# Kernel tuning notes

Hardware: AMD Instinct MI355X
Metric: run time of the kernel (lower is better)

## Reference

```python
import jax, jax.numpy as jnp
import numpy as np

EPS = 1e-5
K = 3  # deformable conv kernel size


def _conv2d_same(x, w, b=None):
    # x (N,C,H,W), w (O,I,kh,kw), stride 1, SAME padding
    y = jax.lax.conv_general_dilated(
        x, w, window_strides=(1, 1), padding='SAME',
        dimension_numbers=('NCHW', 'OIHW', 'NCHW'))
    if b is not None:
        y = y + b[None, :, None, None]
    return y


def _bilinear_sample(x, ys, xs):
    # x (N,C,H,W); ys, xs (N,H,W) float sample coords -> (N,C,H,W), zero pad outside
    N, C, H, W = x.shape
    y0 = jnp.floor(ys)
    x0 = jnp.floor(xs)
    dy = ys - y0
    dx = xs - x0
    xf = x.reshape(N, C, H * W)

    def gather(yi, xi):
        valid = (yi >= 0) & (yi < H) & (xi >= 0) & (xi < W)
        yc = jnp.clip(yi, 0, H - 1).astype(jnp.int32)
        xc = jnp.clip(xi, 0, W - 1).astype(jnp.int32)
        idx = (yc * W + xc).reshape(N, 1, H * W)
        v = jnp.take_along_axis(xf, jnp.broadcast_to(idx, (N, C, H * W)), axis=2)
        return v.reshape(N, C, H, W) * valid[:, None].astype(x.dtype)

    v00 = gather(y0, x0)
    v01 = gather(y0, x0 + 1)
    v10 = gather(y0 + 1, x0)
    v11 = gather(y0 + 1, x0 + 1)
    dy = dy[:, None]
    dx = dx[:, None]
    return (v00 * (1 - dy) * (1 - dx) + v01 * (1 - dy) * dx
            + v10 * dy * (1 - dx) + v11 * dy * dx)


def _dcn_v2(x, w_off, b_off, w, b):
    # Modulated deformable conv (DCNv2), 3x3, stride 1, pad 1
    N, Cin, H, W = x.shape
    om = _conv2d_same(x, w_off, b_off)              # (N, 3*K*K, H, W)
    o1, o2, m = jnp.split(om, 3, axis=1)
    off = jnp.concatenate([o1, o2], axis=1)          # (N, 2*K*K, H, W)
    mask = jax.nn.sigmoid(m)                         # (N, K*K, H, W)
    base_y = jnp.arange(H, dtype=x.dtype)[None, :, None]  # (1,H,1)
    base_x = jnp.arange(W, dtype=x.dtype)[None, None, :]  # (1,1,W)
    out = jnp.broadcast_to(b[None, :, None, None], (N, w.shape[0], H, W)).astype(x.dtype)
    for k in range(K * K):  # fixed small loop over kernel taps
        ki, kj = k // K, k % K
        ys = base_y + (ki - 1) + off[:, 2 * k]
        xs = base_x + (kj - 1) + off[:, 2 * k + 1]
        v = _bilinear_sample(x, ys, xs) * mask[:, k][:, None]
        out = out + jnp.einsum('nchw,oc->nohw', v, w[:, :, ki, kj])
    return out


def _batchnorm(x, gamma, beta):
    # training-mode BN over (N,H,W)
    mu = x.mean(axis=(0, 2, 3), keepdims=True)
    var = x.var(axis=(0, 2, 3), keepdims=True)
    xhat = (x - mu) * jax.lax.rsqrt(var + EPS)
    return xhat * gamma[None, :, None, None] + beta[None, :, None, None]


def _conv_transpose2d(x, w):
    # torch ConvTranspose2d(k=4, s=2, p=1, bias=False); w (Cin, Cout, 4, 4)
    kernel = jnp.flip(w, (2, 3)).transpose(1, 0, 2, 3)  # (Cout, Cin, 4, 4)
    return jax.lax.conv_general_dilated(
        x, kernel, window_strides=(1, 1),
        padding=((2, 2), (2, 2)), lhs_dilation=(2, 2),
        dimension_numbers=('NCHW', 'OIHW', 'NCHW'))


def setup_inputs() -> dict:
    key = jax.random.key(0)
    ks = jax.random.split(key, 9)
    N, inC, outC, H, W = 8, 256, 256, 64, 64
    x = jax.random.normal(ks[0], (N, inC, H, W), dtype=jnp.float32)
    w_off = jax.random.normal(ks[1], (3 * K * K, inC, K, K), dtype=jnp.float32) * 0.01
    b_off = jnp.zeros((3 * K * K,), dtype=jnp.float32)
    w_dcn = jax.random.normal(ks[2], (outC, inC, K, K), dtype=jnp.float32) * (1.0 / np.sqrt(inC * K * K))
    b_dcn = jnp.zeros((outC,), dtype=jnp.float32)
    gamma1 = jnp.ones((outC,), dtype=jnp.float32)
    beta1 = jnp.zeros((outC,), dtype=jnp.float32)
    w_ct = jax.random.normal(ks[3], (outC, outC, 4, 4), dtype=jnp.float32) * (1.0 / np.sqrt(outC * 16))
    gamma2 = jnp.ones((outC,), dtype=jnp.float32)
    beta2 = jnp.zeros((outC,), dtype=jnp.float32)
    return {'x': x, 'w_off': w_off, 'b_off': b_off, 'w_dcn': w_dcn,
            'b_dcn': b_dcn, 'gamma1': gamma1, 'beta1': beta1,
            'w_ct': w_ct, 'gamma2': gamma2, 'beta2': beta2}


def reference(x, w_off, b_off, w_dcn, b_dcn, gamma1, beta1, w_ct, gamma2, beta2):
    out = _dcn_v2(x, w_off, b_off, w_dcn, b_dcn)
    out = jax.nn.relu(_batchnorm(out, gamma1, beta1))
    out = _conv_transpose2d(out, w_ct)
    out = jax.nn.relu(_batchnorm(out, gamma2, beta2))
    return out  # (N, outC, 2H, 2W)
```

## Files before the change

kernel.cpp:

```cpp
#include <hip/hip_runtime.h>


#define OFF_XT   0u
#define SZ_XT    (8u*64u*64u*256u)
#define OFF_Y1   (OFF_XT + SZ_XT)
#define SZ_Y1    SZ_XT
#define OFF_OM   (OFF_Y1 + SZ_Y1)
#define SZ_OM    (8u*27u*4096u)
#define OFF_WD   (OFF_OM + SZ_OM)
#define SZ_WD    (9u*256u*256u)
#define OFF_WC   (OFF_WD + SZ_WD)
#define SZ_WC    (16u*256u*256u)
#define OFF_WO   (OFF_WC + 524288u)
#define OFF_ST   (OFF_WC + SZ_WC)
#define OFF_P1   (OFF_ST + 2048u)

typedef __attribute__((ext_vector_type(8))) short bf16x8;
typedef __attribute__((ext_vector_type(4))) float f32x4;

__device__ __forceinline__ unsigned short f2bf(float f) {
  unsigned int u = __float_as_uint(f);
  u += 0x7fffu + ((u >> 16) & 1u);
  return (unsigned short)(u >> 16);
}

__device__ __forceinline__ unsigned int lerp_pair(unsigned int u00, unsigned int u01,
                                                  unsigned int u10, unsigned int u11,
                                                  float w0, float w1, float w2, float w3) {
  float lo = w0 * __uint_as_float(u00 << 16) + w1 * __uint_as_float(u01 << 16) +
             w2 * __uint_as_float(u10 << 16) + w3 * __uint_as_float(u11 << 16);
  float hi = w0 * __uint_as_float(u00 & 0xffff0000u) + w1 * __uint_as_float(u01 & 0xffff0000u) +
             w2 * __uint_as_float(u10 & 0xffff0000u) + w3 * __uint_as_float(u11 & 0xffff0000u);
  return (unsigned int)f2bf(lo) | ((unsigned int)f2bf(hi) << 16);
}

__global__ __launch_bounds__(256) void k_transpose_x(const float* __restrict__ x,
                                                     unsigned short* __restrict__ xtb) {
  __shared__ float tile[32][33];
  int ny = blockIdx.x;
  int n = ny >> 6, y = ny & 63;
  int c0 = blockIdx.y * 32;
  int w0 = blockIdx.z * 32;
  int t = threadIdx.x;
  int tx = t & 31, ty = t >> 5;
#pragma unroll
  for (int i = 0; i < 4; ++i) {
    int c = c0 + ty + i * 8;
    tile[ty + i * 8][tx] = x[(((n * 256 + c) * 64 + y) << 6) + w0 + tx];
  }
  __syncthreads();
#pragma unroll
  for (int i = 0; i < 4; ++i) {
    int wl = ty + i * 8;
    xtb[(((n * 64 + y) * 64 + (w0 + wl)) << 8) + c0 + tx] = f2bf(tile[tx][wl]);
  }
}

__global__ void k_prep_wdcn(const float* __restrict__ w, unsigned short* __restrict__ wdb) {
  int idx = blockIdx.x * 256 + threadIdx.x;
  if (idx < 589824) {
    int cil = idx & 31;
    int co = (idx >> 5) & 255;
    int chunk = (idx >> 13) & 7;
    int k = idx >> 16;
    int ci = chunk * 32 + cil;
    wdb[idx] = f2bf(w[(co * 256 + ci) * 9 + k]);
  }
}

__global__ void k_prep_wct(const float* __restrict__ w, unsigned short* __restrict__ wcb) {
  int idx = blockIdx.x * 256 + threadIdx.x;
  int cil = idx & 31;
  int co = (idx >> 5) & 255;
  int chunk = (idx >> 13) & 7;
  int tap = (idx >> 16) & 3;
  int px = (idx >> 18) & 1;
  int py = (idx >> 19) & 1;
  int ci = chunk * 32 + cil;
  int krA = (py == 0) ? 3 : 2, krB = (py == 0) ? 1 : 0;
  int kc0 = (px == 0) ? 3 : 2, kc1 = kc0 - 2;
  int kr = (tap < 2) ? krA : krB;
  int kc = (tap & 1) ? kc1 : kc0;
  float v = w[(ci << 12) + (co << 4) + kr * 4 + kc];
  wcb[idx] = f2bf(v);
}

__global__ void k_prep_woff(const float* __restrict__ w, unsigned short* __restrict__ wob) {
  int idx = blockIdx.x * 256 + threadIdx.x;
  int cil = idx & 31;
  int co = (idx >> 5) & 31;
  int chunk = (idx >> 10) & 7;
  int tap = idx >> 13;
  int ci = chunk * 32 + cil;
  float v = (co < 27) ? w[(co * 256 + ci) * 9 + tap] : 0.f;
  wob[idx] = f2bf(v);
}

__global__ __launch_bounds__(512) void k_offset_mfma(const unsigned short* __restrict__ xtb,
                                                     const unsigned short* __restrict__ wob,
                                                     const float* __restrict__ b_off,
                                                     float* __restrict__ om) {
  __shared__ unsigned short aLds[6 * 66 * 40];
  __shared__ unsigned short wLds[9 * 32 * 40];
  int bid = blockIdx.x;
  int n = bid & 7, yq = bid >> 3;
  int ybase = yq * 4;
  int t = threadIdx.x;
  int wave = t >> 6, lane = t & 63;
  int lr = wave >> 1, cb = (wave & 1) * 32;
  int l15 = lane & 15, l4 = lane >> 4;
  f32x4 acc[2][2] = {};

  for (int chunk = 0; chunk < 8; ++chunk) {
    __syncthreads();
    for (int task = t; task < 1584; task += 512) {
      int slot = task & 3;
      int rc = task >> 2;
      int c = rc % 66, r = rc / 66;
      int gy = ybase - 1 + r, gx = c - 1;
      uint4 val = make_uint4(0u, 0u, 0u, 0u);
      if (gy >= 0 && gy < 64 && gx >= 0 && gx < 64)
        val = *(const uint4*)&xtb[((size_t)(n * 4096 + gy * 64 + gx) << 8) + chunk * 32 + slot * 8];
      *(uint4*)&aLds[(r * 66 + c) * 40 + slot * 8] = val;
    }
    for (int task = t; task < 1152; task += 512) {
      int sl = task & 3;
      int co = (task >> 2) & 31;
      int tap = task >> 7;
      *(uint4*)&wLds[(tap * 32 + co) * 40 + sl * 8] =
          *(const uint4*)&wob[(size_t)((tap * 8 + chunk) * 32 + co) * 32 + sl * 8];
    }
    __syncthreads();
#pragma unroll
    for (int ky = 0; ky < 3; ++ky)
#pragma unroll
      for (int kx = 0; kx < 3; ++kx) {
        int tap = ky * 3 + kx;
        bf16x8 b0 = *(bf16x8*)&wLds[(tap * 32 + l15) * 40 + l4 * 8];
        bf16x8 b1 = *(bf16x8*)&wLds[(tap * 32 + 16 + l15) * 40 + l4 * 8];
        bf16x8 a0 = *(bf16x8*)&aLds[((lr + ky) * 66 + cb + l15 + kx) * 40 + l4 * 8];
        bf16x8 a1 = *(bf16x8*)&aLds[((lr + ky) * 66 + cb + 16 + l15 + kx) * 40 + l4 * 8];
        acc[0][0] = __builtin_amdgcn_mfma_f32_16x16x32_bf16(a0, b0, acc[0][0], 0, 0, 0);
        acc[0][1] = __builtin_amdgcn_mfma_f32_16x16x32_bf16(a0, b1, acc[0][1], 0, 0, 0);
        acc[1][0] = __builtin_amdgcn_mfma_f32_16x16x32_bf16(a1, b0, acc[1][0], 0, 0, 0);
        acc[1][1] = __builtin_amdgcn_mfma_f32_16x16x32_bf16(a1, b1, acc[1][1], 0, 0, 0);
      }
  }
  int row = ybase + lr;
#pragma unroll
  for (int j = 0; j < 2; ++j) {
    int co = 16 * j + l15;
    if (co < 27) {
      float bias = b_off[co];
      float* dst = om + ((size_t)(n * 27 + co) << 12) + row * 64;
#pragma unroll
      for (int i = 0; i < 2; ++i) {
        f32x4 v = acc[i][j];
        float4 o = make_float4(v[0] + bias, v[1] + bias, v[2] + bias, v[3] + bias);
        *(float4*)&dst[cb + 16 * i + l4 * 4] = o;
      }
    }
  }
}

__global__ __launch_bounds__(512) void k_dcn2(const unsigned short* __restrict__ xtb,
                                              const float* __restrict__ om,
                                              const unsigned short* __restrict__ wdb,
                                              const float* __restrict__ b_dcn,
                                              unsigned short* __restrict__ y1r,
                                              float* __restrict__ part1) {
  __shared__ unsigned short aLds[128 * 40];
  __shared__ int p_yx[1152];
  __shared__ float p_w[1152 * 4];
  __shared__ float sstat[512];
  int bid = blockIdx.x;
  int n = bid & 7, yp = bid >> 3;
  int ybase = yp * 2;
  int t = threadIdx.x;
  int wave = t >> 6, lane = t & 63;
  int mh = wave >> 2, ns = wave & 3;
  int l15 = lane & 15, l4 = lane >> 4;
  int gp = t >> 2, gq = t & 3;
  int nb = n << 12;
  f32x4 acc[4][4] = {};

  for (int i = t; i < 1152; i += 512) {
    int tap = i >> 7, pp = i & 127;
    int ki = tap / 3, kj = tap % 3;
    int yy = ybase + (pp >> 6), xx = pp & 63;
    const float* base = om + (n * 27) * 4096 + (yy << 6) + xx;
    float offy = base[(2 * tap) * 4096];
    float offx = base[(2 * tap + 1) * 4096];
    float mv = base[(18 + tap) * 4096];
    float mask = 1.f / (1.f + expf(-mv));
    float ysf = (float)(yy + ki - 1) + offy;
    float xsf = (float)(xx + kj - 1) + offx;
    float y0f = floorf(ysf), x0f = floorf(xsf);
    float dy = ysf - y0f, dx = xsf - x0f;
    int y0 = (int)y0f, x0 = (int)x0f;
    int y1c = y0 + 1, x1c = x0 + 1;
    float v00 = (y0 >= 0 && y0 < 64 && x0 >= 0 && x0 < 64) ? 1.f : 0.f;
    float v01 = (y0 >= 0 && y0 < 64 && x1c >= 0 && x1c < 64) ? 1.f : 0.f;
    float v10 = (y1c >= 0 && y1c < 64 && x0 >= 0 && x0 < 64) ? 1.f : 0.f;
    float v11 = (y1c >= 0 && y1c < 64 && x1c >= 0 && x1c < 64) ? 1.f : 0.f;
    int cy0 = min(max(y0, 0), 63), cy1 = min(max(y1c, 0), 63);
    int cx0 = min(max(x0, 0), 63), cx1 = min(max(x1c, 0), 63);
    p_yx[i] = cy0 | (cy1 << 8) | (cx0 << 16) | (cx1 << 24);
    p_w[i * 4 + 0] = (1.f - dy) * (1.f - dx) * mask * v00;
    p_w[i * 4 + 1] = (1.f - dy) * dx * mask * v01;
    p_w[i * 4 + 2] = dy * (1.f - dx) * mask * v10;
    p_w[i * 4 + 3] = dy * dx * mask * v11;
  }
  __syncthreads();

  const unsigned short *b00, *b01, *b10, *b11;
  float w0, w1, w2, w3;
#define LOADP(TAP_)                                                                   \
  {                                                                                   \
    int ii = (TAP_) * 128 + gp;                                                       \
    int pk = p_yx[ii];                                                                \
    int y0 = pk & 255, y1c = (pk >> 8) & 255, x0 = (pk >> 16) & 255, x1c = pk >> 24;  \
    w0 = p_w[ii * 4 + 0]; w1 = p_w[ii * 4 + 1];                                       \
    w2 = p_w[ii * 4 + 2]; w3 = p_w[ii * 4 + 3];                                       \
    b00 = xtb + ((size_t)(nb + (y0 << 6) + x0) << 8) + gq * 8;                        \
    b01 = xtb + ((size_t)(nb + (y0 << 6) + x1c) << 8) + gq * 8;                       \
    b10 = xtb + ((size_t)(nb + (y1c << 6) + x0) << 8) + gq * 8;                       \
    b11 = xtb + ((size_t)(nb + (y1c << 6) + x1c) << 8) + gq * 8;                      \
  }
  uint4 g00, g01, g10, g11;
  LOADP(0);
  g00 = *(const uint4*)(b00); g01 = *(const uint4*)(b01);
  g10 = *(const uint4*)(b10); g11 = *(const uint4*)(b11);

  for (int tap = 0; tap < 9; ++tap) {
    for (int chunk = 0; chunk < 8; ++chunk) {
      __syncthreads();
      {
        uint4 o;
        o.x = lerp_pair(g00.x, g01.x, g10.x, g11.x, w0, w1, w2, w3);
        o.y = lerp_pair(g00.y, g01.y, g10.y, g11.y, w0, w1, w2, w3);
        o.z = lerp_pair(g00.z, g01.z, g10.z, g11.z, w0, w1, w2, w3);
        o.w = lerp_pair(g00.w, g01.w, g10.w, g11.w, w0, w1, w2, w3);
        *(uint4*)&aLds[gp * 40 + gq * 8] = o;
      }
      if (!(tap == 8 && chunk == 7)) {
        int ntap = tap, nchunk = chunk + 1;
        if (nchunk == 8) { nchunk = 0; ntap = tap + 1; LOADP(ntap); }
        int cio = nchunk * 32;
        g00 = *(const uint4*)(b00 + cio); g01 = *(const uint4*)(b01 + cio);
        g10 = *(const uint4*)(b10 + cio); g11 = *(const uint4*)(b11 + cio);
      }
      __syncthreads();
      const unsigned short* wp = wdb + (size_t)tap * 65536 + chunk * 8192;
      bf16x8 b[4], a[4];
#pragma unroll
      for (int j = 0; j < 4; ++j)
        b[j] = *(bf16x8*)&wp[(ns * 64 + 16 * j + l15) * 32 + l4 * 8];
#pragma unroll
      for (int i = 0; i < 4; ++i)
        a[i] = *(bf16x8*)&aLds[(mh * 64 + 16 * i + l15) * 40 + l4 * 8];
#pragma unroll
      for (int i = 0; i < 4; ++i)
#pragma unroll
        for (int j = 0; j < 4; ++j)
          acc[i][j] = __builtin_amdgcn_mfma_f32_16x16x32_bf16(a[i], b[j], acc[i][j], 0, 0, 0);
    }
  }
#undef LOADP
  sstat[t] = 0.f;
  __syncthreads();
  unsigned short* dst = y1r + ((size_t)(n * 4096 + ybase * 64) << 8);
#pragma unroll
  for (int j = 0; j < 4; ++j) {
    int co = ns * 64 + 16 * j + l15;
    float bias = b_dcn[co];
    float ss = 0.f, qq = 0.f;
#pragma unroll
    for (int i = 0; i < 4; ++i)
#pragma unroll
      for (int rr = 0; rr < 4; ++rr) {
        int pos = mh * 64 + 16 * i + l4 * 4 + rr;
        float v = acc[i][j][rr] + bias;
        dst[pos * 256 + co] = f2bf(v);
        ss += v; qq += v * v;
      }
    ss += __shfl_xor(ss, 16); ss += __shfl_xor(ss, 32);
    qq += __shfl_xor(qq, 16); qq += __shfl_xor(qq, 32);
    if (l4 == 0) { atomicAdd(&sstat[co], ss); atomicAdd(&sstat[256 + co], qq); }
  }
  __syncthreads();
  part1[(size_t)bid * 512 + t] = sstat[t];
}

__global__ __launch_bounds__(256) void k_finalize_p(const float* __restrict__ part,
                                                    const float* __restrict__ gamma,
                                                    const float* __restrict__ beta,
                                                    float* __restrict__ scsh,
                                                    float inv_cnt, int nblocks) {
  __shared__ float red[512];
  int c = blockIdx.x;
  int t = threadIdx.x;
  float s = 0.f, q = 0.f;
  for (int b = t; b < nblocks; b += 256) {
    s += part[(size_t)b * 512 + c];
    q += part[(size_t)b * 512 + 256 + c];
  }
  red[t] = s;
  red[256 + t] = q;
  __syncthreads();
  for (int w = 128; w > 0; w >>= 1) {
    if (t < w) { red[t] += red[t + w]; red[256 + t] += red[256 + t + w]; }
    __syncthreads();
  }
  if (t == 0) {
    float mu = red[0] * inv_cnt;
    float var = red[256] * inv_cnt - mu * mu;
    float r = rsqrtf(var + 1e-5f);
    float sc = gamma[c] * r;
    scsh[c] = sc;
    scsh[256 + c] = beta[c] - mu * sc;
  }
}

__global__ void k_norm_b16(unsigned short* __restrict__ y1r, const float* __restrict__ scsh) {
  int idx = blockIdx.x * 256 + threadIdx.x;
  int cb = (idx & 31) * 8;
  uint4 v = *(uint4*)&y1r[(size_t)idx * 8];
  float4 sc0 = *(const float4*)&scsh[cb];
  float4 sc1 = *(const float4*)&scsh[cb + 4];
  float4 sh0 = *(const float4*)&scsh[256 + cb];
  float4 sh1 = *(const float4*)&scsh[256 + cb + 4];
  float f0 = __uint_as_float(v.x << 16), f1 = __uint_as_float(v.x & 0xffff0000u);
  float f2 = __uint_as_float(v.y << 16), f3 = __uint_as_float(v.y & 0xffff0000u);
  float f4 = __uint_as_float(v.z << 16), f5 = __uint_as_float(v.z & 0xffff0000u);
  float f6 = __uint_as_float(v.w << 16), f7 = __uint_as_float(v.w & 0xffff0000u);
  f0 = fmaxf(fmaf(f0, sc0.x, sh0.x), 0.f); f1 = fmaxf(fmaf(f1, sc0.y, sh0.y), 0.f);
  f2 = fmaxf(fmaf(f2, sc0.z, sh0.z), 0.f); f3 = fmaxf(fmaf(f3, sc0.w, sh0.w), 0.f);
  f4 = fmaxf(fmaf(f4, sc1.x, sh1.x), 0.f); f5 = fmaxf(fmaf(f5, sc1.y, sh1.y), 0.f);
  f6 = fmaxf(fmaf(f6, sc1.z, sh1.z), 0.f); f7 = fmaxf(fmaf(f7, sc1.w, sh1.w), 0.f);
  uint4 o;
  o.x = (unsigned int)f2bf(f0) | ((unsigned int)f2bf(f1) << 16);
  o.y = (unsigned int)f2bf(f2) | ((unsigned int)f2bf(f3) << 16);
  o.z = (unsigned int)f2bf(f4) | ((unsigned int)f2bf(f5) << 16);
  o.w = (unsigned int)f2bf(f6) | ((unsigned int)f2bf(f7) << 16);
  *(uint4*)&y1r[(size_t)idx * 8] = o;
}

__global__ __launch_bounds__(512) void k_convt2(const unsigned short* __restrict__ y1b,
                                               const unsigned short* __restrict__ wcb,
                                               float* __restrict__ out,
                                               float* __restrict__ part2) {
  __shared__ unsigned short sh[16896];
  __shared__ float sstat[512];
  unsigned short* aLds = sh;

  int bid = blockIdx.x;
  int n = bid & 7;
  int r2 = bid >> 3;
  int py = r2 & 1;
  int ub = r2 >> 1;
  int u0 = ub * 2;
  int ry0 = u0 - 1 + py;
  int t = threadIdx.x;
  int wave = t >> 6, lane = t & 63;
  int px_w = wave >> 2, ns = wave & 3;
  int co_base = ns * 64;
  int l15 = lane & 15, l4 = lane >> 4;
  bool rvalid[3];
#pragma unroll
  for (int r = 0; r < 3; ++r) rvalid[r] = (ry0 + r >= 0) && (ry0 + r < 64);

  f32x4 acc[2][4][4] = {};

  for (int chunk = 0; chunk < 8; ++chunk) {
    int ci0 = chunk * 32;
    __syncthreads();
    for (int task = t; task < 792; task += 512) {
      int slot = task & 3;
      int rc = task >> 2;
      int c = rc % 66;
      int r = rc / 66;
      int ix = c - 1;
      uint4 val = make_uint4(0u, 0u, 0u, 0u);
      if (rvalid[r] && ix >= 0 && ix < 64)
        val = *(const uint4*)&y1b[((size_t)(n * 4096 + (ry0 + r) * 64 + ix) * 256 + ci0 + slot * 8)];
      *(uint4*)&aLds[(r * 66 + c) * 40 + slot * 8] = val;
    }
    __syncthreads();
    for (int tap = 0; tap < 4; ++tap) {
      int r_ofs = tap >> 1, s = tap & 1;
      const unsigned short* wsrc =
          wcb + ((size_t)((((py * 2 + px_w) * 4 + tap) * 8 + chunk) * 256 + co_base)) * 32;
      bf16x8 b[4];
#pragma unroll
      for (int j = 0; j < 4; ++j)
        b[j] = *(bf16x8*)&wsrc[(16 * j + l15) * 32 + l4 * 8];
#pragma unroll
      for (int k = 0; k < 2; ++k)
#pragma unroll
        for (int i = 0; i < 4; ++i) {
          int c = 16 * i + l15 + s + px_w;
          bf16x8 a = *(bf16x8*)&aLds[((k + r_ofs) * 66 + c) * 40 + l4 * 8];
#pragma unroll
          for (int j = 0; j < 4; ++j)
            acc[k][i][j] = __builtin_amdgcn_mfma_f32_16x16x32_bf16(a, b[j], acc[k][i][j], 0, 0, 0);
        }
    }
  }

  sstat[t] = 0.f;
  float* epi = (float*)sh;
#pragma unroll
  for (int k = 0; k < 2; ++k) {
    int oy = 2 * (u0 + k) + py;
    for (int qt = 0; qt < 4; ++qt) {
      __syncthreads();
      if (ns == qt) {
#pragma unroll
        for (int i = 0; i < 4; ++i)
#pragma unroll
          for (int j = 0; j < 4; ++j) {
            int co_l = 16 * j + l15;
            int vbase = 16 * i + l4 * 4;
            *(f32x4*)&epi[co_l * 132 + px_w * 64 + vbase] = acc[k][i][j];
          }
      }
      __syncthreads();
#pragma unroll
      for (int it = 0; it < 4; ++it) {
        int task = it * 512 + t;
        int q = task & 31;
        int co_l = task >> 5;
        int co = qt * 64 + co_l;
        float e00 = epi[co_l * 132 + 2 * q];
        float e01 = epi[co_l * 132 + 2 * q + 1];
        float e10 = epi[co_l * 132 + 64 + 2 * q];
        float e11 = epi[co_l * 132 + 64 + 2 * q + 1];
        float4 vv = make_float4(e00, e10, e01, e11);
        *(float4*)&out[((size_t)(n * 256 + co) * 128 + oy) * 128 + 4 * q] = vv;
        float ss = e00 + e01 + e10 + e11;
        float qq = e00 * e00 + e01 * e01 + e10 * e10 + e11 * e11;
        ss += __shfl_xor(ss, 1);  qq += __shfl_xor(qq, 1);
        ss += __shfl_xor(ss, 2);  qq += __shfl_xor(qq, 2);
        ss += __shfl_xor(ss, 4);  qq += __shfl_xor(qq, 4);
        ss += __shfl_xor(ss, 8);  qq += __shfl_xor(qq, 8);
        ss += __shfl_xor(ss, 16); qq += __shfl_xor(qq, 16);
        if ((lane & 31) == 0) {
          atomicAdd(&sstat[co], ss);
          atomicAdd(&sstat[256 + co], qq);
        }
      }
    }
  }
  __syncthreads();
  part2[(size_t)bid * 512 + t] = sstat[t];
}

__global__ void k_norm_nchw(float* __restrict__ buf, const float* __restrict__ scsh) {
  int idx = blockIdx.x * 256 + threadIdx.x;
  int c = (idx >> 12) & 255;
  float sc = scsh[c], sh = scsh[256 + c];
  float4 v = *(float4*)&buf[(size_t)idx * 4];
  v.x = fmaxf(fmaf(v.x, sc, sh), 0.f);
  v.y = fmaxf(fmaf(v.y, sc, sh), 0.f);
  v.z = fmaxf(fmaf(v.z, sc, sh), 0.f);
  v.w = fmaxf(fmaf(v.w, sc, sh), 0.f);
  *(float4*)&buf[(size_t)idx * 4] = v;
}

extern "C" void kernel_launch(void* const* d_in, const int* in_sizes, int n_in,
                              void* d_out, int out_size, void* d_ws, size_t ws_size,
                              hipStream_t stream) {
  (void)in_sizes; (void)n_in; (void)out_size; (void)ws_size;
  const float* x      = (const float*)d_in[0];
  const float* w_off  = (const float*)d_in[1];
  const float* b_off  = (const float*)d_in[2];
  const float* w_dcn  = (const float*)d_in[3];
  const float* b_dcn  = (const float*)d_in[4];
  const float* gamma1 = (const float*)d_in[5];
  const float* beta1  = (const float*)d_in[6];
  const float* w_ct   = (const float*)d_in[7];
  const float* gamma2 = (const float*)d_in[8];
  const float* beta2  = (const float*)d_in[9];
  float* ws  = (float*)d_ws;
  unsigned short* xtb = (unsigned short*)(ws + OFF_XT);
  unsigned short* y1r = (unsigned short*)(ws + OFF_Y1);
  float* om  = ws + OFF_OM;
  unsigned short* wdb = (unsigned short*)(ws + OFF_WD);
  unsigned short* wcb = (unsigned short*)(ws + OFF_WC);
  unsigned short* wob = (unsigned short*)(ws + OFF_WO);
  float* st  = ws + OFF_ST;
  float* p1  = ws + OFF_P1;
  float* out = (float*)d_out;

  k_transpose_x<<<dim3(512, 8, 2), 256, 0, stream>>>(x, xtb);
  k_prep_wdcn<<<2304, 256, 0, stream>>>(w_dcn, wdb);
  k_prep_wct<<<4096, 256, 0, stream>>>(w_ct, wcb);
  k_prep_woff<<<288, 256, 0, stream>>>(w_off, wob);
  k_offset_mfma<<<128, 512, 0, stream>>>(xtb, wob, b_off, om);
  k_dcn2<<<256, 512, 0, stream>>>(xtb, om, wdb, b_dcn, y1r, p1);
  k_finalize_p<<<256, 256, 0, stream>>>(p1, gamma1, beta1, st + 512, 1.f / 32768.f, 256);
  k_norm_b16<<<4096, 256, 0, stream>>>(y1r, st + 512);
  k_convt2<<<512, 512, 0, stream>>>(y1r, wcb, out, om);
  k_finalize_p<<<256, 256, 0, stream>>>(om, gamma2, beta2, st + 1536, 1.f / 131072.f, 512);
  k_norm_nchw<<<32768, 256, 0, stream>>>(out, st + 1536);
}
```

Before: 281.5 us.

## Fuse BN1+ReLU into convT loader and halve DCN block rows

Removes the separate k_norm_b16 pass by applying BN1 scale/shift and ReLU while k_convt2 loads y1 into LDS. k_dcn2 now handles one output row per block instead of two, doubling the grid to 512 blocks with smaller tiles and 8-byte gathers per thread. The partial-stats buffer is relocated to fit the larger block count. This saves a full read/write pass over the bf16 intermediate and raises parallelism in the DCN kernel, at the cost of less weight reuse per block and redundant normalization math across halo rows in the convT loader.

```diff
diff --git a/kernel.cpp b/kernel.cpp
--- a/kernel.cpp
+++ b/kernel.cpp
@@ -12,8 +12,8 @@
 #define OFF_WC   (OFF_WD + SZ_WD)
 #define SZ_WC    (16u*256u*256u)
 #define OFF_WO   (OFF_WC + 524288u)
+#define OFF_P1   (OFF_WC + 565248u)
 #define OFF_ST   (OFF_WC + SZ_WC)
-#define OFF_P1   (OFF_ST + 2048u)
 
 typedef __attribute__((ext_vector_type(8))) short bf16x8;
 typedef __attribute__((ext_vector_type(4))) float f32x4;
@@ -31,6 +31,13 @@
              w2 * __uint_as_float(u10 << 16) + w3 * __uint_as_float(u11 << 16);
   float hi = w0 * __uint_as_float(u00 & 0xffff0000u) + w1 * __uint_as_float(u01 & 0xffff0000u) +
              w2 * __uint_as_float(u10 & 0xffff0000u) + w3 * __uint_as_float(u11 & 0xffff0000u);
+  return (unsigned int)f2bf(lo) | ((unsigned int)f2bf(hi) << 16);
+}
+
+__device__ __forceinline__ unsigned int norm_pair(unsigned int u, float scx, float shx,
+                                                  float scy, float shy) {
+  float lo = fmaxf(fmaf(__uint_as_float(u << 16), scx, shx), 0.f);
+  float hi = fmaxf(fmaf(__uint_as_float(u & 0xffff0000u), scy, shy), 0.f);
   return (unsigned int)f2bf(lo) | ((unsigned int)f2bf(hi) << 16);
 }
 
@@ -169,32 +176,30 @@
                                               const float* __restrict__ b_dcn,
                                               unsigned short* __restrict__ y1r,
                                               float* __restrict__ part1) {
-  __shared__ unsigned short aLds[128 * 40];
-  __shared__ int p_yx[1152];
-  __shared__ float p_w[1152 * 4];
+  __shared__ unsigned short aLds[64 * 40];
+  __shared__ int p_yx[576];
+  __shared__ float p_w[576 * 4];
   __shared__ float sstat[512];
   int bid = blockIdx.x;
-  int n = bid & 7, yp = bid >> 3;
-  int ybase = yp * 2;
+  int n = bid & 7, y = bid >> 3;
   int t = threadIdx.x;
   int wave = t >> 6, lane = t & 63;
   int mh = wave >> 2, ns = wave & 3;
   int l15 = lane & 15, l4 = lane >> 4;
-  int gp = t >> 2, gq = t & 3;
+  int gp = t >> 3, gq = t & 7;
   int nb = n << 12;
-  f32x4 acc[4][4] = {};
-
-  for (int i = t; i < 1152; i += 512) {
-    int tap = i >> 7, pp = i & 127;
+  f32x4 acc[2][4] = {};
+
+  for (int i = t; i < 576; i += 512) {
+    int tap = i >> 6, pp = i & 63;
     int ki = tap / 3, kj = tap % 3;
-    int yy = ybase + (pp >> 6), xx = pp & 63;
-    const float* base = om + (n * 27) * 4096 + (yy << 6) + xx;
+    const float* base = om + (n * 27) * 4096 + (y << 6) + pp;
     float offy = base[(2 * tap) * 4096];
     float offx = base[(2 * tap + 1) * 4096];
     float mv = base[(18 + tap) * 4096];
     float mask = 1.f / (1.f + expf(-mv));
-    float ysf = (float)(yy + ki - 1) + offy;
-    float xsf = (float)(xx + kj - 1) + offx;
+    float ysf = (float)(y + ki - 1) + offy;
+    float xsf = (float)(pp + kj - 1) + offx;
     float y0f = floorf(ysf), x0f = floorf(xsf);
     float dy = ysf - y0f, dx = xsf - x0f;
     int y0 = (int)y0f, x0 = (int)x0f;
@@ -217,50 +222,48 @@
   float w0, w1, w2, w3;
 #define LOADP(TAP_)                                                                   \
   {                                                                                   \
-    int ii = (TAP_) * 128 + gp;                                                       \
+    int ii = (TAP_) * 64 + gp;                                                        \
     int pk = p_yx[ii];                                                                \
     int y0 = pk & 255, y1c = (pk >> 8) & 255, x0 = (pk >> 16) & 255, x1c = pk >> 24;  \
     w0 = p_w[ii * 4 + 0]; w1 = p_w[ii * 4 + 1];                                       \
     w2 = p_w[ii * 4 + 2]; w3 = p_w[ii * 4 + 3];                                       \
-    b00 = xtb + ((size_t)(nb + (y0 << 6) + x0) << 8) + gq * 8;                        \
-    b01 = xtb + ((size_t)(nb + (y0 << 6) + x1c) << 8) + gq * 8;                       \
-    b10 = xtb + ((size_t)(nb + (y1c << 6) + x0) << 8) + gq * 8;                       \
-    b11 = xtb + ((size_t)(nb + (y1c << 6) + x1c) << 8) + gq * 8;                      \
-  }
-  uint4 g00, g01, g10, g11;
+    b00 = xtb + ((size_t)(nb + (y0 << 6) + x0) << 8) + gq * 4;                        \
+    b01 = xtb + ((size_t)(nb + (y0 << 6) + x1c) << 8) + gq * 4;                       \
+    b10 = xtb + ((size_t)(nb + (y1c << 6) + x0) << 8) + gq * 4;                       \
+    b11 = xtb + ((size_t)(nb + (y1c << 6) + x1c) << 8) + gq * 4;                      \
+  }
+  uint2 g00, g01, g10, g11;
   LOADP(0);
-  g00 = *(const uint4*)(b00); g01 = *(const uint4*)(b01);
-  g10 = *(const uint4*)(b10); g11 = *(const uint4*)(b11);
+  g00 = *(const uint2*)(b00); g01 = *(const uint2*)(b01);
+  g10 = *(const uint2*)(b10); g11 = *(const uint2*)(b11);
 
   for (int tap = 0; tap < 9; ++tap) {
     for (int chunk = 0; chunk < 8; ++chunk) {
       __syncthreads();
       {
-        uint4 o;
+        uint2 o;
         o.x = lerp_pair(g00.x, g01.x, g10.x, g11.x, w0, w1, w2, w3);
         o.y = lerp_pair(g00.y, g01.y, g10.y, g11.y, w0, w1, w2, w3);
-        o.z = lerp_pair(g00.z, g01.z, g10.z, g11.z, w0, w1, w2, w3);
-        o.w = lerp_pair(g00.w, g01.w, g10.w, g11.w, w0, w1, w2, w3);
-        *(uint4*)&aLds[gp * 40 + gq * 8] = o;
+        *(uint2*)&aLds[gp * 40 + gq * 4] = o;
       }
       if (!(tap == 8 && chunk == 7)) {
         int ntap = tap, nchunk = chunk + 1;
         if (nchunk == 8) { nchunk = 0; ntap = tap + 1; LOADP(ntap); }
         int cio = nchunk * 32;
-        g00 = *(const uint4*)(b00 + cio); g01 = *(const uint4*)(b01 + cio);
-        g10 = *(const uint4*)(b10 + cio); g11 = *(const uint4*)(b11 + cio);
+        g00 = *(const uint2*)(b00 + cio); g01 = *(const uint2*)(b01 + cio);
+        g10 = *(const uint2*)(b10 + cio); g11 = *(const uint2*)(b11 + cio);
       }
       __syncthreads();
       const unsigned short* wp = wdb + (size_t)tap * 65536 + chunk * 8192;
-      bf16x8 b[4], a[4];
+      bf16x8 b[4], a[2];
 #pragma unroll
       for (int j = 0; j < 4; ++j)
         b[j] = *(bf16x8*)&wp[(ns * 64 + 16 * j + l15) * 32 + l4 * 8];
 #pragma unroll
-      for (int i = 0; i < 4; ++i)
-        a[i] = *(bf16x8*)&aLds[(mh * 64 + 16 * i + l15) * 40 + l4 * 8];
-#pragma unroll
-      for (int i = 0; i < 4; ++i)
+      for (int i = 0; i < 2; ++i)
+        a[i] = *(bf16x8*)&aLds[(mh * 32 + 16 * i + l15) * 40 + l4 * 8];
+#pragma unroll
+      for (int i = 0; i < 2; ++i)
 #pragma unroll
         for (int j = 0; j < 4; ++j)
           acc[i][j] = __builtin_amdgcn_mfma_f32_16x16x32_bf16(a[i], b[j], acc[i][j], 0, 0, 0);
@@ -269,17 +272,17 @@
 #undef LOADP
   sstat[t] = 0.f;
   __syncthreads();
-  unsigned short* dst = y1r + ((size_t)(n * 4096 + ybase * 64) << 8);
+  unsigned short* dst = y1r + ((size_t)(n * 4096 + y * 64) << 8);
 #pragma unroll
   for (int j = 0; j < 4; ++j) {
     int co = ns * 64 + 16 * j + l15;
     float bias = b_dcn[co];
     float ss = 0.f, qq = 0.f;
 #pragma unroll
-    for (int i = 0; i < 4; ++i)
+    for (int i = 0; i < 2; ++i)
 #pragma unroll
       for (int rr = 0; rr < 4; ++rr) {
-        int pos = mh * 64 + 16 * i + l4 * 4 + rr;
+        int pos = mh * 32 + 16 * i + l4 * 4 + rr;
         float v = acc[i][j][rr] + bias;
         dst[pos * 256 + co] = f2bf(v);
         ss += v; qq += v * v;
@@ -322,32 +325,9 @@
   }
 }
 
-__global__ void k_norm_b16(unsigned short* __restrict__ y1r, const float* __restrict__ scsh) {
-  int idx = blockIdx.x * 256 + threadIdx.x;
-  int cb = (idx & 31) * 8;
-  uint4 v = *(uint4*)&y1r[(size_t)idx * 8];
-  float4 sc0 = *(const float4*)&scsh[cb];
-  float4 sc1 = *(const float4*)&scsh[cb + 4];
-  float4 sh0 = *(const float4*)&scsh[256 + cb];
-  float4 sh1 = *(const float4*)&scsh[256 + cb + 4];
-  float f0 = __uint_as_float(v.x << 16), f1 = __uint_as_float(v.x & 0xffff0000u);
-  float f2 = __uint_as_float(v.y << 16), f3 = __uint_as_float(v.y & 0xffff0000u);
-  float f4 = __uint_as_float(v.z << 16), f5 = __uint_as_float(v.z & 0xffff0000u);
-  float f6 = __uint_as_float(v.w << 16), f7 = __uint_as_float(v.w & 0xffff0000u);
-  f0 = fmaxf(fmaf(f0, sc0.x, sh0.x), 0.f); f1 = fmaxf(fmaf(f1, sc0.y, sh0.y), 0.f);
-  f2 = fmaxf(fmaf(f2, sc0.z, sh0.z), 0.f); f3 = fmaxf(fmaf(f3, sc0.w, sh0.w), 0.f);
-  f4 = fmaxf(fmaf(f4, sc1.x, sh1.x), 0.f); f5 = fmaxf(fmaf(f5, sc1.y, sh1.y), 0.f);
-  f6 = fmaxf(fmaf(f6, sc1.z, sh1.z), 0.f); f7 = fmaxf(fmaf(f7, sc1.w, sh1.w), 0.f);
-  uint4 o;
-  o.x = (unsigned int)f2bf(f0) | ((unsigned int)f2bf(f1) << 16);
-  o.y = (unsigned int)f2bf(f2) | ((unsigned int)f2bf(f3) << 16);
-  o.z = (unsigned int)f2bf(f4) | ((unsigned int)f2bf(f5) << 16);
-  o.w = (unsigned int)f2bf(f6) | ((unsigned int)f2bf(f7) << 16);
-  *(uint4*)&y1r[(size_t)idx * 8] = o;
-}
-
 __global__ __launch_bounds__(512) void k_convt2(const unsigned short* __restrict__ y1b,
                                                const unsigned short* __restrict__ wcb,
+                                               const float* __restrict__ scsh1,
                                                float* __restrict__ out,
                                                float* __restrict__ part2) {
   __shared__ unsigned short sh[16896];
@@ -382,8 +362,18 @@
       int r = rc / 66;
       int ix = c - 1;
       uint4 val = make_uint4(0u, 0u, 0u, 0u);
-      if (rvalid[r] && ix >= 0 && ix < 64)
-        val = *(const uint4*)&y1b[((size_t)(n * 4096 + (ry0 + r) * 64 + ix) * 256 + ci0 + slot * 8)];
+      if (rvalid[r] && ix >= 0 && ix < 64) {
+        uint4 raw = *(const uint4*)&y1b[((size_t)(n * 4096 + (ry0 + r) * 64 + ix) * 256 + ci0 + slot * 8)];
+        int cb = ci0 + slot * 8;
+        float4 sc0 = *(const float4*)&scsh1[cb];
+        float4 sc1 = *(const float4*)&scsh1[cb + 4];
+        float4 sh0 = *(const float4*)&scsh1[256 + cb];
+        float4 sh1 = *(const float4*)&scsh1[256 + cb + 4];
+        val.x = norm_pair(raw.x, sc0.x, sh0.x, sc0.y, sh0.y);
+        val.y = norm_pair(raw.y, sc0.z, sh0.z, sc0.w, sh0.w);
+        val.z = norm_pair(raw.z, sc1.x, sh1.x, sc1.y, sh1.y);
+        val.w = norm_pair(raw.w, sc1.z, sh1.z, sc1.w, sh1.w);
+      }
       *(uint4*)&aLds[(r * 66 + c) * 40 + slot * 8] = val;
     }
     __syncthreads();
@@ -498,10 +488,9 @@
   k_prep_wct<<<4096, 256, 0, stream>>>(w_ct, wcb);
   k_prep_woff<<<288, 256, 0, stream>>>(w_off, wob);
   k_offset_mfma<<<128, 512, 0, stream>>>(xtb, wob, b_off, om);
-  k_dcn2<<<256, 512, 0, stream>>>(xtb, om, wdb, b_dcn, y1r, p1);
-  k_finalize_p<<<256, 256, 0, stream>>>(p1, gamma1, beta1, st + 512, 1.f / 32768.f, 256);
-  k_norm_b16<<<4096, 256, 0, stream>>>(y1r, st + 512);
-  k_convt2<<<512, 512, 0, stream>>>(y1r, wcb, out, om);
+  k_dcn2<<<512, 512, 0, stream>>>(xtb, om, wdb, b_dcn, y1r, p1);
+  k_finalize_p<<<256, 256, 0, stream>>>(p1, gamma1, beta1, st + 512, 1.f / 32768.f, 512);
+  k_convt2<<<512, 512, 0, stream>>>(y1r, wcb, st + 512, out, om);
   k_finalize_p<<<256, 256, 0, stream>>>(om, gamma2, beta2, st + 1536, 1.f / 131072.f, 512);
   k_norm_nchw<<<32768, 256, 0, stream>>>(out, st + 1536);
 }
```

After: 294.2 us. 4.5% more time.

## Double-buffer DCN A tile and fuse BN1+ReLU into conv-transpose loads

Applied to the files above, without the earlier changes.

Gives the DCN GEMM's A tile two LDS buffers, so each step computes the next bilinear tile while MFMAs consume the current one, dropping one barrier per iteration. Removes the standalone BN1+ReLU kernel and applies scale, shift and ReLU while loading y1 into LDS in the conv-transpose kernel. This saves a full read and write pass over the y1 intermediate and a launch, but repeats the normalisation for rows shared between the overlapping tiles. The P1 partial buffer is moved to a new workspace offset.

```diff
diff --git a/kernel.cpp b/kernel.cpp
--- a/kernel.cpp
+++ b/kernel.cpp
@@ -12,8 +12,8 @@
 #define OFF_WC   (OFF_WD + SZ_WD)
 #define SZ_WC    (16u*256u*256u)
 #define OFF_WO   (OFF_WC + 524288u)
+#define OFF_P1   (OFF_WC + 565248u)
 #define OFF_ST   (OFF_WC + SZ_WC)
-#define OFF_P1   (OFF_ST + 2048u)
 
 typedef __attribute__((ext_vector_type(8))) short bf16x8;
 typedef __attribute__((ext_vector_type(4))) float f32x4;
@@ -31,6 +31,13 @@
              w2 * __uint_as_float(u10 << 16) + w3 * __uint_as_float(u11 << 16);
   float hi = w0 * __uint_as_float(u00 & 0xffff0000u) + w1 * __uint_as_float(u01 & 0xffff0000u) +
              w2 * __uint_as_float(u10 & 0xffff0000u) + w3 * __uint_as_float(u11 & 0xffff0000u);
+  return (unsigned int)f2bf(lo) | ((unsigned int)f2bf(hi) << 16);
+}
+
+__device__ __forceinline__ unsigned int norm_pair(unsigned int u, float scx, float shx,
+                                                  float scy, float shy) {
+  float lo = fmaxf(fmaf(__uint_as_float(u << 16), scx, shx), 0.f);
+  float hi = fmaxf(fmaf(__uint_as_float(u & 0xffff0000u), scy, shy), 0.f);
   return (unsigned int)f2bf(lo) | ((unsigned int)f2bf(hi) << 16);
 }
 
@@ -169,7 +176,7 @@
                                               const float* __restrict__ b_dcn,
                                               unsigned short* __restrict__ y1r,
                                               float* __restrict__ part1) {
-  __shared__ unsigned short aLds[128 * 40];
+  __shared__ unsigned short aLds[2][128 * 40];
   __shared__ int p_yx[1152];
   __shared__ float p_w[1152 * 4];
   __shared__ float sstat[512];
@@ -227,46 +234,55 @@
     b10 = xtb + ((size_t)(nb + (y1c << 6) + x0) << 8) + gq * 8;                       \
     b11 = xtb + ((size_t)(nb + (y1c << 6) + x1c) << 8) + gq * 8;                      \
   }
+#define WRITE_A(BUF_)                                                                 \
+  {                                                                                   \
+    uint4 o;                                                                          \
+    o.x = lerp_pair(g00.x, g01.x, g10.x, g11.x, w0, w1, w2, w3);                      \
+    o.y = lerp_pair(g00.y, g01.y, g10.y, g11.y, w0, w1, w2, w3);                      \
+    o.z = lerp_pair(g00.z, g01.z, g10.z, g11.z, w0, w1, w2, w3);                      \
+    o.w = lerp_pair(g00.w, g01.w, g10.w, g11.w, w0, w1, w2, w3);                      \
+    *(uint4*)&aLds[BUF_][gp * 40 + gq * 8] = o;                                       \
+  }
   uint4 g00, g01, g10, g11;
   LOADP(0);
   g00 = *(const uint4*)(b00); g01 = *(const uint4*)(b01);
   g10 = *(const uint4*)(b10); g11 = *(const uint4*)(b11);
-
-  for (int tap = 0; tap < 9; ++tap) {
-    for (int chunk = 0; chunk < 8; ++chunk) {
-      __syncthreads();
-      {
-        uint4 o;
-        o.x = lerp_pair(g00.x, g01.x, g10.x, g11.x, w0, w1, w2, w3);
-        o.y = lerp_pair(g00.y, g01.y, g10.y, g11.y, w0, w1, w2, w3);
-        o.z = lerp_pair(g00.z, g01.z, g10.z, g11.z, w0, w1, w2, w3);
-        o.w = lerp_pair(g00.w, g01.w, g10.w, g11.w, w0, w1, w2, w3);
-        *(uint4*)&aLds[gp * 40 + gq * 8] = o;
-      }
-      if (!(tap == 8 && chunk == 7)) {
-        int ntap = tap, nchunk = chunk + 1;
-        if (nchunk == 8) { nchunk = 0; ntap = tap + 1; LOADP(ntap); }
-        int cio = nchunk * 32;
+  WRITE_A(0);
+  g00 = *(const uint4*)(b00 + 32); g01 = *(const uint4*)(b01 + 32);
+  g10 = *(const uint4*)(b10 + 32); g11 = *(const uint4*)(b11 + 32);
+  __syncthreads();
+
+  for (int p = 0; p < 72; ++p) {
+    int cur = p & 1;
+    int tap = p >> 3, chunk = p & 7;
+    const unsigned short* wp = wdb + (size_t)tap * 65536 + chunk * 8192;
+    bf16x8 b[4], a[4];
+#pragma unroll
+    for (int j = 0; j < 4; ++j)
+      b[j] = *(bf16x8*)&wp[(ns * 64 + 16 * j + l15) * 32 + l4 * 8];
+#pragma unroll
+    for (int i = 0; i < 4; ++i)
+      a[i] = *(bf16x8*)&aLds[cur][(mh * 64 + 16 * i + l15) * 40 + l4 * 8];
+#pragma unroll
+    for (int i = 0; i < 4; ++i)
+#pragma unroll
+      for (int j = 0; j < 4; ++j)
+        acc[i][j] = __builtin_amdgcn_mfma_f32_16x16x32_bf16(a[i], b[j], acc[i][j], 0, 0, 0);
+    if (p < 71) {
+      WRITE_A(cur ^ 1);
+      int q = p + 2;
+      if (q < 72) {
+        int qt = q >> 3, qc = q & 7;
+        if (qc == 0) LOADP(qt);
+        int cio = qc * 32;
         g00 = *(const uint4*)(b00 + cio); g01 = *(const uint4*)(b01 + cio);
         g10 = *(const uint4*)(b10 + cio); g11 = *(const uint4*)(b11 + cio);
       }
-      __syncthreads();
-      const unsigned short* wp = wdb + (size_t)tap * 65536 + chunk * 8192;
-      bf16x8 b[4], a[4];
-#pragma unroll
-      for (int j = 0; j < 4; ++j)
-        b[j] = *(bf16x8*)&wp[(ns * 64 + 16 * j + l15) * 32 + l4 * 8];
-#pragma unroll
-      for (int i = 0; i < 4; ++i)
-        a[i] = *(bf16x8*)&aLds[(mh * 64 + 16 * i + l15) * 40 + l4 * 8];
-#pragma unroll
-      for (int i = 0; i < 4; ++i)
-#pragma unroll
-        for (int j = 0; j < 4; ++j)
-          acc[i][j] = __builtin_amdgcn_mfma_f32_16x16x32_bf16(a[i], b[j], acc[i][j], 0, 0, 0);
-    }
+    }
+    __syncthreads();
   }
 #undef LOADP
+#undef WRITE_A
   sstat[t] = 0.f;
   __syncthreads();
   unsigned short* dst = y1r + ((size_t)(n * 4096 + ybase * 64) << 8);
@@ -322,32 +338,9 @@
   }
 }
 
-__global__ void k_norm_b16(unsigned short* __restrict__ y1r, const float* __restrict__ scsh) {
-  int idx = blockIdx.x * 256 + threadIdx.x;
-  int cb = (idx & 31) * 8;
-  uint4 v = *(uint4*)&y1r[(size_t)idx * 8];
-  float4 sc0 = *(const float4*)&scsh[cb];
-  float4 sc1 = *(const float4*)&scsh[cb + 4];
-  float4 sh0 = *(const float4*)&scsh[256 + cb];
-  float4 sh1 = *(const float4*)&scsh[256 + cb + 4];
-  float f0 = __uint_as_float(v.x << 16), f1 = __uint_as_float(v.x & 0xffff0000u);
-  float f2 = __uint_as_float(v.y << 16), f3 = __uint_as_float(v.y & 0xffff0000u);
-  float f4 = __uint_as_float(v.z << 16), f5 = __uint_as_float(v.z & 0xffff0000u);
-  float f6 = __uint_as_float(v.w << 16), f7 = __uint_as_float(v.w & 0xffff0000u);
-  f0 = fmaxf(fmaf(f0, sc0.x, sh0.x), 0.f); f1 = fmaxf(fmaf(f1, sc0.y, sh0.y), 0.f);
-  f2 = fmaxf(fmaf(f2, sc0.z, sh0.z), 0.f); f3 = fmaxf(fmaf(f3, sc0.w, sh0.w), 0.f);
-  f4 = fmaxf(fmaf(f4, sc1.x, sh1.x), 0.f); f5 = fmaxf(fmaf(f5, sc1.y, sh1.y), 0.f);
-  f6 = fmaxf(fmaf(f6, sc1.z, sh1.z), 0.f); f7 = fmaxf(fmaf(f7, sc1.w, sh1.w), 0.f);
-  uint4 o;
-  o.x = (unsigned int)f2bf(f0) | ((unsigned int)f2bf(f1) << 16);
-  o.y = (unsigned int)f2bf(f2) | ((unsigned int)f2bf(f3) << 16);
-  o.z = (unsigned int)f2bf(f4) | ((unsigned int)f2bf(f5) << 16);
-  o.w = (unsigned int)f2bf(f6) | ((unsigned int)f2bf(f7) << 16);
-  *(uint4*)&y1r[(size_t)idx * 8] = o;
-}
-
 __global__ __launch_bounds__(512) void k_convt2(const unsigned short* __restrict__ y1b,
                                                const unsigned short* __restrict__ wcb,
+                                               const float* __restrict__ scsh1,
                                                float* __restrict__ out,
                                                float* __restrict__ part2) {
   __shared__ unsigned short sh[16896];
@@ -382,8 +375,18 @@
       int r = rc / 66;
       int ix = c - 1;
       uint4 val = make_uint4(0u, 0u, 0u, 0u);
-      if (rvalid[r] && ix >= 0 && ix < 64)
-        val = *(const uint4*)&y1b[((size_t)(n * 4096 + (ry0 + r) * 64 + ix) * 256 + ci0 + slot * 8)];
+      if (rvalid[r] && ix >= 0 && ix < 64) {
+        uint4 raw = *(const uint4*)&y1b[((size_t)(n * 4096 + (ry0 + r) * 64 + ix) * 256 + ci0 + slot * 8)];
+        int cb = ci0 + slot * 8;
+        float4 sc0 = *(const float4*)&scsh1[cb];
+        float4 sc1 = *(const float4*)&scsh1[cb + 4];
+        float4 sh0 = *(const float4*)&scsh1[256 + cb];
+        float4 sh1 = *(const float4*)&scsh1[256 + cb + 4];
+        val.x = norm_pair(raw.x, sc0.x, sh0.x, sc0.y, sh0.y);
+        val.y = norm_pair(raw.y, sc0.z, sh0.z, sc0.w, sh0.w);
+        val.z = norm_pair(raw.z, sc1.x, sh1.x, sc1.y, sh1.y);
+        val.w = norm_pair(raw.w, sc1.z, sh1.z, sc1.w, sh1.w);
+      }
       *(uint4*)&aLds[(r * 66 + c) * 40 + slot * 8] = val;
     }
     __syncthreads();
@@ -500,8 +503,7 @@
   k_offset_mfma<<<128, 512, 0, stream>>>(xtb, wob, b_off, om);
   k_dcn2<<<256, 512, 0, stream>>>(xtb, om, wdb, b_dcn, y1r, p1);
   k_finalize_p<<<256, 256, 0, stream>>>(p1, gamma1, beta1, st + 512, 1.f / 32768.f, 256);
-  k_norm_b16<<<4096, 256, 0, stream>>>(y1r, st + 512);
-  k_convt2<<<512, 512, 0, stream>>>(y1r, wcb, out, om);
+  k_convt2<<<512, 512, 0, stream>>>(y1r, wcb, st + 512, out, om);
   k_finalize_p<<<256, 256, 0, stream>>>(om, gamma2, beta2, st + 1536, 1.f / 131072.f, 512);
   k_norm_nchw<<<32768, 256, 0, stream>>>(out, st + 1536);
 }
```

Measured after the change: 257.0 us. 8.7% less time.
